# Optimization experiments

Measured on AMD Instinct MI355X. Metric: run time of the kernel, lower is better.

## Reference

```python
import jax, jax.numpy as jnp
import numpy as np
from jax import lax

B, C, H, W = 64, 512, 14, 14
HEAD_DIM = 32
NUM_HEADS = C // HEAD_DIM
HIDDEN = int(C * 4.0)
EPS = 1e-5
LS_INIT = 1e-5


def setup_inputs() -> dict:
    key = jax.random.key(0)
    ks = jax.random.split(key, 16)
    d = {}
    d['x'] = jax.random.normal(ks[0], (B, C, H, W), dtype=jnp.float32)
    # shared BatchNorm2d(dim) (inference-mode, running stats)
    d['bn_g'] = 1.0 + 0.1 * jax.random.normal(ks[1], (C,), dtype=jnp.float32)
    d['bn_b'] = 0.1 * jax.random.normal(ks[2], (C,), dtype=jnp.float32)
    d['bn_m'] = 0.1 * jax.random.normal(ks[3], (C,), dtype=jnp.float32)
    d['bn_v'] = jax.random.uniform(ks[4], (C,), minval=0.5, maxval=1.5, dtype=jnp.float32)
    # MHSA params (qkv_bias=False)
    d['qkv_w'] = 0.02 * jax.random.normal(ks[5], (3 * C, C), dtype=jnp.float32)
    d['proj_w'] = 0.02 * jax.random.normal(ks[6], (C, C), dtype=jnp.float32)
    d['proj_b'] = jnp.zeros((C,), dtype=jnp.float32)
    # ConvFFN: depthwise 7x7 (groups=C, no bias) -> BN -> 1x1 -> GELU -> 1x1
    d['dw_w'] = 0.02 * jax.random.normal(ks[7], (C, 1, 7, 7), dtype=jnp.float32)
    d['fbn_g'] = 1.0 + 0.1 * jax.random.normal(ks[8], (C,), dtype=jnp.float32)
    d['fbn_b'] = 0.1 * jax.random.normal(ks[9], (C,), dtype=jnp.float32)
    d['fbn_m'] = 0.1 * jax.random.normal(ks[10], (C,), dtype=jnp.float32)
    d['fbn_v'] = jax.random.uniform(ks[11], (C,), minval=0.5, maxval=1.5, dtype=jnp.float32)
    d['fc1_w'] = 0.02 * jax.random.normal(ks[12], (HIDDEN, C), dtype=jnp.float32)
    d['fc1_b'] = jnp.zeros((HIDDEN,), dtype=jnp.float32)
    d['fc2_w'] = 0.02 * jax.random.normal(ks[13], (C, HIDDEN), dtype=jnp.float32)
    d['fc2_b'] = jnp.zeros((C,), dtype=jnp.float32)
    # layer scale params, shape (C,1,1)
    d['ls1'] = LS_INIT * jnp.ones((C, 1, 1), dtype=jnp.float32)
    d['ls2'] = LS_INIT * jnp.ones((C, 1, 1), dtype=jnp.float32)
    return d


def _bn2d(x, g, b, m, v):
    # inference BatchNorm2d over channel dim of NCHW
    inv = g * lax.rsqrt(v + EPS)
    return x * inv[None, :, None, None] + (b - m * inv)[None, :, None, None]


def _mhsa(x, qkv_w, proj_w, proj_b):
    b, c, h, w = x.shape
    n = h * w
    xt = x.reshape(b, c, n).transpose(0, 2, 1)              # [B,N,C]
    qkv = xt @ qkv_w.T                                       # [B,N,3C]
    qkv = qkv.reshape(b, n, 3, NUM_HEADS, HEAD_DIM).transpose(2, 0, 3, 1, 4)
    q, k, v = qkv[0], qkv[1], qkv[2]                         # [B,h,N,d]
    scale = HEAD_DIM ** -0.5
    attn = jax.nn.softmax(jnp.einsum('bhnd,bhmd->bhnm', q * scale, k), axis=-1)
    o = jnp.einsum('bhnm,bhmd->bhnd', attn, v)               # [B,h,N,d]
    o = o.transpose(0, 2, 1, 3).reshape(b, n, c)             # [B,N,C]
    o = o @ proj_w.T + proj_b
    return o.transpose(0, 2, 1).reshape(b, c, h, w)


def _convffn(x, dw_w, fbn_g, fbn_b, fbn_m, fbn_v, fc1_w, fc1_b, fc2_w, fc2_b):
    y = lax.conv_general_dilated(x, dw_w, window_strides=(1, 1),
                                 padding=[(3, 3), (3, 3)],
                                 feature_group_count=C,
                                 dimension_numbers=('NCHW', 'OIHW', 'NCHW'))
    y = _bn2d(y, fbn_g, fbn_b, fbn_m, fbn_v)
    y = jnp.einsum('bchw,oc->bohw', y, fc1_w) + fc1_b[None, :, None, None]
    y = jax.nn.gelu(y, approximate=False)
    y = jnp.einsum('bchw,oc->bohw', y, fc2_w) + fc2_b[None, :, None, None]
    return y


def reference(x, bn_g, bn_b, bn_m, bn_v, qkv_w, proj_w, proj_b,
              dw_w, fbn_g, fbn_b, fbn_m, fbn_v, fc1_w, fc1_b, fc2_w, fc2_b,
              ls1, ls2):
    xn = _bn2d(x, bn_g, bn_b, bn_m, bn_v)
    x = x + ls1[None] * _mhsa(xn, qkv_w, proj_w, proj_b)
    xn = _bn2d(x, bn_g, bn_b, bn_m, bn_v)
    x = x + ls2[None] * _convffn(xn, dw_w, fbn_g, fbn_b, fbn_m, fbn_v,
                                 fc1_w, fc1_b, fc2_w, fc2_b)
    return x
```

## Files before the change

### kernel.cpp

```cpp
#include <hip/hip_runtime.h>
#include <hip/hip_bf16.h>
#include <hip/hip_fp8.h>
#include <stdint.h>

#define NTOK 196
#define NB   64
#define CCH  512
#define HID  2048
#define MTOT (NB * NTOK)

typedef __attribute__((ext_vector_type(8))) short  short8v;
typedef __attribute__((ext_vector_type(4))) float  float4v;
typedef __attribute__((ext_vector_type(2))) int    int2v;


__device__ __forceinline__ void mfma_fp8(float4v& d, int2v a, int2v b) {
  asm("v_mfma_f32_16x16x32_fp8_fp8 %0, %1, %2, %0" : "+v"(d) : "v"(a), "v"(b));
}

__device__ __forceinline__ void gload_lds16(const void* gsrc, void* ldst) {
  __builtin_amdgcn_global_load_lds(
      (const __attribute__((address_space(1))) unsigned int*)gsrc,
      (__attribute__((address_space(3))) unsigned int*)ldst, 16, 0, 0);
}

__device__ __forceinline__ int swz4(int r) { return (r ^ (r >> 2)) & 3; }

__device__ __forceinline__ uint32_t cvt2_fp8(float a, float b) {
  uint32_t d;
  asm("v_cvt_pk_fp8_f32 %0, %1, %2" : "=v"(d) : "v"(a), "v"(b));
  return d;
}


__global__ void prep_consts(const float* __restrict__ bn_g, const float* __restrict__ bn_b,
                            const float* __restrict__ bn_m, const float* __restrict__ bn_v,
                            const float* __restrict__ fbn_g, const float* __restrict__ fbn_b,
                            const float* __restrict__ fbn_m, const float* __restrict__ fbn_v,
                            float* __restrict__ cst) {
  int c = blockIdx.x * blockDim.x + threadIdx.x;
  if (c < CCH) {
    float i1 = bn_g[c] * rsqrtf(bn_v[c] + 1e-5f);
    cst[c] = i1;
    cst[512 + c] = bn_b[c] - bn_m[c] * i1;
    float i2 = fbn_g[c] * rsqrtf(fbn_v[c] + 1e-5f);
    cst[1024 + c] = i2;
    cst[1536 + c] = fbn_b[c] - fbn_m[c] * i2;
  }
}


__global__ void cvt_weights(const float* __restrict__ qkv_w, const float* __restrict__ proj_w,
                            const float* __restrict__ fc1_w, const float* __restrict__ fc2_w,
                            uint8_t* __restrict__ qkvb, uint8_t* __restrict__ projb,
                            uint8_t* __restrict__ fc1b, uint8_t* __restrict__ fc2b) {
  int i4 = blockIdx.x * blockDim.x + threadIdx.x;
  const int nq = 1536 * 512 / 4;
  const int np = 512 * 512 / 4;
  const int n1 = 2048 * 512 / 4;
  const float* src;
  uint8_t* dst;
  int k;
  if (i4 < nq)                { src = qkv_w;  dst = qkvb;  k = i4; }
  else if (i4 < nq + np)      { src = proj_w; dst = projb; k = i4 - nq; }
  else if (i4 < nq + np + n1) { src = fc1_w;  dst = fc1b;  k = i4 - nq - np; }
  else                        { src = fc2_w;  dst = fc2b;  k = i4 - nq - np - n1; }
  float4v v = *(const float4v*)(src + 4 * (size_t)k);
  uint32_t w0 = cvt2_fp8(v[0] * 16.0f, v[1] * 16.0f);
  uint32_t w1 = cvt2_fp8(v[2] * 16.0f, v[3] * 16.0f);
  *(uint16_t*)(dst + 4 * (size_t)k)     = (uint16_t)w0;
  *(uint16_t*)(dst + 4 * (size_t)k + 2) = (uint16_t)w1;
}


__global__ __launch_bounds__(256) void transpose_x(
    const float* __restrict__ x, uint8_t* __restrict__ xnt8,
    __hip_bfloat16* __restrict__ xt, const float* __restrict__ cst) {
  __shared__ float tile[32][33];
  const int n0 = blockIdx.x * 32;
  const int c0 = blockIdx.y * 32;
  const int b  = blockIdx.z;
  const int j = threadIdx.x & 31, i = threadIdx.x >> 5;
  #pragma unroll
  for (int p = 0; p < 4; ++p) {
    int cc = c0 + i + p * 8;
    int n = n0 + j;
    if (n < NTOK) tile[i + p * 8][j] = x[((size_t)b * CCH + cc) * NTOK + n];
  }
  __syncthreads();
  const float s = cst[c0 + j], t = cst[512 + c0 + j];
  float bn[4];
  size_t off[4];
  bool ok[4];
  #pragma unroll
  for (int p = 0; p < 4; ++p) {
    int n = n0 + i + p * 8;
    int cc = c0 + j;
    ok[p] = (n < NTOK);
    if (ok[p]) {
      float raw = tile[j][i + p * 8];
      size_t o = ((size_t)b * NTOK + n) * CCH + cc;
      xt[o] = __float2bfloat16(raw);
      bn[p] = raw * s + t;
      off[p] = o;
    }
  }
  uint32_t w0 = cvt2_fp8(bn[0], bn[1]);
  uint32_t w1 = cvt2_fp8(bn[2], bn[3]);
  if (ok[0]) xnt8[off[0]] = (uint8_t)w0;
  if (ok[1]) xnt8[off[1]] = (uint8_t)(w0 >> 8);
  if (ok[2]) xnt8[off[2]] = (uint8_t)w1;
  if (ok[3]) xnt8[off[3]] = (uint8_t)(w1 >> 8);
}


template<int EPI>
__global__ __launch_bounds__(256, 3) void gemm8f(
    const uint8_t* __restrict__ A, const uint8_t* __restrict__ Bw,
    int N, int K, int NY,
    __hip_bfloat16* __restrict__ outb, uint8_t* __restrict__ out8,
    const float* __restrict__ bias, const float* __restrict__ ls,
    const __hip_bfloat16* __restrict__ resid) {
  __shared__ char lds[49152];
  const int tid  = threadIdx.x;
  const int lane = tid & 63;
  const int wave = tid >> 6;

  const int q    = (int)gridDim.x >> 3;
  const int orig = blockIdx.x;
  const int wgid = (orig & 7) * q + (orig >> 3);
  const int bx = wgid / NY;
  const int by = wgid - bx * NY;

  const int m0 = bx * 128;
  const int n0 = by * 128;
  const int wm = (wave >> 1) * 64;
  const int wn = (wave & 1) * 64;
  const int KT = K >> 6;

  float4v acc[4][4] = {};

  auto stage = [&](int buf, int kt) {
    const int kb = kt * 64;
    char* base = lds + buf * 16384;
    #pragma unroll
    for (int i = 0; i < 2; ++i) {
      int L = i * 4096 + tid * 16;
      int row = L >> 6;
      int lc = ((L >> 4) & 3) ^ swz4(row);
      gload_lds16(A + (size_t)(m0 + row) * K + kb + lc * 16, base + L);
    }
    #pragma unroll
    for (int i = 0; i < 2; ++i) {
      int L = i * 4096 + tid * 16;
      int row = L >> 6;
      int lc = ((L >> 4) & 3) ^ swz4(row);
      gload_lds16(Bw + (size_t)(n0 + row) * K + kb + lc * 16, base + 8192 + L);
    }
  };

  auto compute = [&](int buf) {
    const char* bA = lds + buf * 16384;
    const char* bB = bA + 8192;
    const int g = lane >> 4;
    #pragma unroll
    for (int t = 0; t < 2; ++t) {
      int2v av[4], bv[4];
      #pragma unroll
      for (int f = 0; f < 4; ++f) {
        int row = wm + f * 16 + (lane & 15);
        int c16 = ((t << 1) | (g >> 1)) ^ swz4(row);
        av[f] = *(const int2v*)(bA + row * 64 + c16 * 16 + (g & 1) * 8);
      }
      #pragma unroll
      for (int j = 0; j < 4; ++j) {
        int row = wn + j * 16 + (lane & 15);
        int c16 = ((t << 1) | (g >> 1)) ^ swz4(row);
        bv[j] = *(const int2v*)(bB + row * 64 + c16 * 16 + (g & 1) * 8);
      }
      #pragma unroll
      for (int i = 0; i < 4; ++i)
        #pragma unroll
        for (int j = 0; j < 4; ++j)
          mfma_fp8(acc[i][j], av[i], bv[j]);
    }
  };

  stage(0, 0);
  stage(1, 1);
  int cur = 0;
  for (int kt = 0; kt < KT - 1; ++kt) {
    asm volatile("s_waitcnt vmcnt(4)" ::: "memory");
    __builtin_amdgcn_s_barrier();
    __builtin_amdgcn_sched_barrier(0);
    if (kt + 2 < KT) {
      int s = cur + 2; if (s >= 3) s -= 3;
      stage(s, kt + 2);
    }
    compute(cur);
    ++cur; if (cur == 3) cur = 0;
  }
  asm volatile("s_waitcnt vmcnt(0)" ::: "memory");
  __builtin_amdgcn_s_barrier();
  __builtin_amdgcn_sched_barrier(0);
  compute(cur);
  asm volatile("s_nop 7\n\ts_nop 7");

  const float RS = 0.0625f;

  if (EPI == 0) {
    #pragma unroll
    for (int i = 0; i < 4; ++i)
      #pragma unroll
      for (int j = 0; j < 4; ++j)
        #pragma unroll
        for (int r = 0; r < 4; r += 2) {
          int m = m0 + wm + i * 16 + ((lane >> 4) << 2) + r;
          int n = n0 + wn + j * 16 + (lane & 15);
          int bb = m / NTOK, tok = m - bb * NTOK;
          int bb2 = (m + 1) / NTOK, tok2 = (m + 1) - bb2 * NTOK;
          int sel = n >> 9, hh = (n >> 5) & 15, d = n & 31;
          uint32_t w = cvt2_fp8(acc[i][j][r] * RS, acc[i][j][r + 1] * RS);
          out8[(((size_t)(sel * 16 + hh) * NB + bb) * NTOK + tok) * 32 + d]  = (uint8_t)w;
          out8[(((size_t)(sel * 16 + hh) * NB + bb2) * NTOK + tok2) * 32 + d] = (uint8_t)(w >> 8);
        }
  } else {
    #pragma unroll
    for (int i = 0; i < 4; ++i)
      #pragma unroll
      for (int j = 0; j < 4; ++j)
        #pragma unroll
        for (int r = 0; r < 4; ++r) {
          int m = m0 + wm + i * 16 + ((lane >> 4) << 2) + r;
          int n = n0 + wn + j * 16 + (lane & 15);
          float v = acc[i][j][r] * RS + bias[n];
          v = __bfloat162float(resid[(size_t)m * CCH + n]) + ls[n] * v;
          outb[(size_t)m * CCH + n] = __float2bfloat16(v);
        }
  }
}


__global__ __launch_bounds__(512, 1) void ffn_fused(
    const uint8_t* __restrict__ yt8, const uint8_t* __restrict__ w1,
    const uint8_t* __restrict__ w2, const float* __restrict__ b1,
    const float* __restrict__ b2, const float* __restrict__ ls2,
    const __hip_bfloat16* __restrict__ resid, float* __restrict__ outf) {
  __shared__ char lds[131072];
  char* sA = lds;
  char* sH = lds + 32768;
  char* sB = lds + 65536;
  const int tid  = threadIdx.x;
  const int lane = tid & 63;
  const int wv   = tid >> 6;
  const int g    = lane >> 4;
  const int l15  = lane & 15;
  const int m0   = blockIdx.x * 64;
  const float RS = 0.0625f;

  #pragma unroll
  for (int u = 0; u < 4; ++u) {
    int L = u * 8192 + tid * 16;
    int r = L >> 9;
    int pc = (L >> 4) & 31;
    int lc = pc ^ (r & 31);
    gload_lds16(yt8 + (size_t)(m0 + r) * 512 + lc * 16, sA + L);
  }

  auto stageB = [&](const uint8_t* W, int rs, int kb, int buf) {
    char* base = sB + buf * 32768;
    #pragma unroll
    for (int u = 0; u < 4; ++u) {
      int L = u * 8192 + tid * 16;
      int r = L >> 6;
      int pc = (L >> 4) & 3;
      int lc = pc ^ swz4(r);
      gload_lds16(W + (size_t)r * rs + kb + lc * 16, base + L);
    }
  };

  auto step = [&](const char* Asrc, int ks, int buf, float4v (&acc)[4][4]) {
    const char* bB = sB + buf * 32768;
    #pragma unroll
    for (int t = 0; t < 2; ++t) {
      int2v av[4], bv[4];
      #pragma unroll
      for (int f = 0; f < 4; ++f) {
        int r = f * 16 + l15;
        int c = ks * 4 + t * 2 + (g >> 1);
        int pc = c ^ (r & 31);
        av[f] = *(const int2v*)(Asrc + r * 512 + pc * 16 + (g & 1) * 8);
      }
      #pragma unroll
      for (int j = 0; j < 4; ++j) {
        int r = wv * 64 + j * 16 + l15;
        int c16 = ((t << 1) | (g >> 1)) ^ swz4(r);
        bv[j] = *(const int2v*)(bB + r * 64 + c16 * 16 + (g & 1) * 8);
      }
      #pragma unroll
      for (int f = 0; f < 4; ++f)
        #pragma unroll
        for (int j = 0; j < 4; ++j)
          mfma_fp8(acc[f][j], av[f], bv[j]);
    }
  };

  float4v acc2[4][4] = {};

  stageB(w1, 512, 0, 0);
  __syncthreads();
  int par = 0;

  #pragma unroll 1
  for (int nh = 0; nh < 4; ++nh) {
    const uint8_t* W1c = w1 + (size_t)nh * 512 * 512;
    float4v acc1[4][4] = {};
    #pragma unroll 1
    for (int ks = 0; ks < 8; ++ks) {
      if (ks < 7) stageB(W1c, 512, (ks + 1) * 64, par ^ 1);
      else        stageB(w2, 2048, nh * 512, par ^ 1);
      step(sA, ks, par, acc1);
      __syncthreads();
      par ^= 1;
    }
    #pragma unroll
    for (int i = 0; i < 4; ++i)
      #pragma unroll
      for (int j = 0; j < 4; ++j) {
        int n = wv * 64 + j * 16 + l15;
        float bias1 = b1[nh * 512 + n];
        #pragma unroll
        for (int r = 0; r < 4; r += 2) {
          int m = i * 16 + (g << 2) + r;
          float z0 = acc1[i][j][r] * RS + bias1;
          float z1 = acc1[i][j][r + 1] * RS + bias1;
          float g0 = z0 / (1.0f + __expf(-1.702f * z0));
          float g1 = z1 / (1.0f + __expf(-1.702f * z1));
          uint32_t w = cvt2_fp8(g0, g1);
          int pc0 = ((n >> 4) ^ (m & 31)) * 16 + (n & 15);
          int pc1 = ((n >> 4) ^ ((m + 1) & 31)) * 16 + (n & 15);
          sH[m * 512 + pc0]       = (uint8_t)w;
          sH[(m + 1) * 512 + pc1] = (uint8_t)(w >> 8);
        }
      }
    __syncthreads();
    #pragma unroll 1
    for (int ks = 0; ks < 8; ++ks) {
      if (ks < 7)      stageB(w2, 2048, nh * 512 + (ks + 1) * 64, par ^ 1);
      else if (nh < 3) stageB(w1 + (size_t)(nh + 1) * 512 * 512, 512, 0, par ^ 1);
      step(sH, ks, par, acc2);
      __syncthreads();
      par ^= 1;
    }
  }
  asm volatile("s_nop 7\n\ts_nop 7");

  #pragma unroll 1
  for (int p = 0; p < 2; ++p) {
    __syncthreads();
    if ((wv >> 2) == p) {
      float* LT = (float*)(lds + (wv & 3) * 17408);
      #pragma unroll
      for (int i = 0; i < 4; ++i)
        #pragma unroll
        for (int j = 0; j < 4; ++j)
          #pragma unroll
          for (int r = 0; r < 4; ++r) {
            int ml = i * 16 + (g << 2) + r;
            int nl = j * 16 + l15;
            int n2 = wv * 64 + nl;
            float v = acc2[i][j][r] * RS + b2[n2];
            v = __bfloat162float(resid[(size_t)(m0 + ml) * CCH + n2]) + ls2[n2] * v;
            LT[nl * 68 + ml] = v;
          }
    }
    __syncthreads();
    #pragma unroll
    for (int u = 0; u < 8; ++u) {
      int idx = tid + 512 * u;
      int s = idx >> 10;
      int nl = (idx >> 4) & 63;
      int mq = idx & 15;
      const float* LT = (const float*)(lds + s * 17408);
      float4v v4 = *(const float4v*)(LT + nl * 68 + mq * 4);
      int n2 = (p * 4 + s) * 64 + nl;
      int m = m0 + mq * 4;
      int bb = m / NTOK, tok = m - bb * NTOK;
      *(float4v*)(outf + (size_t)bb * (CCH * NTOK) + (size_t)n2 * NTOK + tok) = v4;
    }
  }
}


__global__ __launch_bounds__(256, 3) void attn_kernel(
    const uint8_t* __restrict__ qkv8, uint8_t* __restrict__ o_t8) {
  __shared__ char sQ[208 * 48];
  __shared__ char sK[224 * 48];
  __shared__ char sV[32 * 240];
  __shared__ char sP[4][16 * 232];
  const int tid  = threadIdx.x;
  const int lane = tid & 63;
  const int wave = tid >> 6;
  const int b = blockIdx.x >> 4;
  const int h = blockIdx.x & 15;
  const size_t CHB = 6272;
  const uint8_t* Qg = qkv8 + ((size_t)(0 * 16 + h) * NB + b) * CHB;
  const uint8_t* Kg = qkv8 + ((size_t)(1 * 16 + h) * NB + b) * CHB;
  const uint8_t* Vg = qkv8 + ((size_t)(2 * 16 + h) * NB + b) * CHB;

  for (int i = tid; i < 144; i += 256) {
    int r = i / 12, w = i % 12;
    ((uint32_t*)(sQ + (196 + r) * 48))[w] = 0u;
  }
  for (int i = tid; i < 336; i += 256) {
    int r = i / 12, w = i % 12;
    ((uint32_t*)(sK + (196 + r) * 48))[w] = 0u;
  }
  for (int i = tid; i < 352; i += 256) {
    int d = i / 11, w = i % 11;
    ((uint32_t*)(sV + d * 240 + 196))[w] = 0u;
  }

  for (int c = tid; c < 392; c += 256) {
    int row = c >> 1, hf = c & 1;
    uint4 vq = *(const uint4*)(Qg + c * 16);
    *(uint4*)(sQ + row * 48 + hf * 16) = vq;
    uint4 vk = *(const uint4*)(Kg + c * 16);
    *(uint4*)(sK + row * 48 + hf * 16) = vk;
  }
  for (int u = tid; u < 784; u += 256) {
    int row = u >> 2, d0 = (u & 3) * 8;
    uint64_t w = *(const uint64_t*)(Vg + (size_t)u * 8);
    #pragma unroll
    for (int e = 0; e < 8; ++e)
      sV[(d0 + e) * 240 + row] = (char)(w >> (8 * e));
  }
  __syncthreads();

  const float scale = 0.17677669529663687f;
  char* Pw = sP[wave];
  const int g = lane >> 4;

  for (int mt = wave; mt < 13; mt += 4) {
    int qrow = mt * 16 + (lane & 15);
    int2v aq = *(const int2v*)(sQ + qrow * 48 + g * 8);

    float4v s[14];
    #pragma unroll
    for (int nt = 0; nt < 14; ++nt) {
      int krow = nt * 16 + (lane & 15);
      int2v bk = *(const int2v*)(sK + krow * 48 + g * 8);
      s[nt] = float4v{0.f, 0.f, 0.f, 0.f};
      mfma_fp8(s[nt], aq, bk);
    }
    asm volatile("s_nop 7\n\ts_nop 7");

    float mx[4] = {-INFINITY, -INFINITY, -INFINITY, -INFINITY};
    #pragma unroll
    for (int nt = 0; nt < 14; ++nt) {
      bool valid = (nt * 16 + (lane & 15)) < NTOK;
      #pragma unroll
      for (int r = 0; r < 4; ++r) {
        float v = valid ? s[nt][r] * scale : -INFINITY;
        s[nt][r] = v;
        mx[r] = fmaxf(mx[r], v);
      }
    }
    #pragma unroll
    for (int off = 1; off < 16; off <<= 1) {
      #pragma unroll
      for (int r = 0; r < 4; ++r) mx[r] = fmaxf(mx[r], __shfl_xor(mx[r], off));
    }
    float sum[4] = {0.f, 0.f, 0.f, 0.f};
    #pragma unroll
    for (int nt = 0; nt < 14; ++nt) {
      #pragma unroll
      for (int r = 0; r < 4; ++r) {
        float e = __expf(s[nt][r] - mx[r]);
        s[nt][r] = e;
        sum[r] += e;
      }
    }
    #pragma unroll
    for (int off = 1; off < 16; off <<= 1) {
      #pragma unroll
      for (int r = 0; r < 4; ++r) sum[r] += __shfl_xor(sum[r], off);
    }
    float rs[4];
    #pragma unroll
    for (int r = 0; r < 4; ++r) rs[r] = 1.0f / sum[r];

    #pragma unroll
    for (int nt = 0; nt < 14; ++nt) {
      int col = nt * 16 + (lane & 15);
      #pragma unroll
      for (int r = 0; r < 4; r += 2) {
        int prow = ((lane >> 4) << 2) + r;
        uint32_t w = cvt2_fp8(s[nt][r], s[nt][r + 1]);
        *(uint8_t*)(Pw + prow * 232 + col)       = (uint8_t)w;
        *(uint8_t*)(Pw + (prow + 1) * 232 + col) = (uint8_t)(w >> 8);
      }
    }

    float4v o0 = float4v{0.f, 0.f, 0.f, 0.f};
    float4v o1 = float4v{0.f, 0.f, 0.f, 0.f};
    #pragma unroll
    for (int ks = 0; ks < 7; ++ks) {
      int2v pa = *(const int2v*)(Pw + (lane & 15) * 232 + ks * 32 + g * 8);
      int2v v0 = *(const int2v*)(sV + (lane & 15) * 240 + ks * 32 + g * 8);
      int2v v1 = *(const int2v*)(sV + (16 + (lane & 15)) * 240 + ks * 32 + g * 8);
      mfma_fp8(o0, pa, v0);
      mfma_fp8(o1, pa, v1);
    }
    asm volatile("s_nop 7\n\ts_nop 7");

    #pragma unroll
    for (int r = 0; r < 4; ++r) {
      int trow = mt * 16 + ((lane >> 4) << 2) + r;
      if (trow < NTOK) {
        size_t ob = ((size_t)b * NTOK + trow) * CCH + h * 32 + (lane & 15);
        uint32_t w = cvt2_fp8(o0[r] * rs[r], o1[r] * rs[r]);
        o_t8[ob]      = (uint8_t)w;
        o_t8[ob + 16] = (uint8_t)(w >> 8);
      }
    }
  }
}


__global__ __launch_bounds__(448) void dwconv_tm(
    const __hip_bfloat16* __restrict__ x1t, const float* __restrict__ dw_w,
    const float* __restrict__ cst, uint8_t* __restrict__ yt8) {
  __shared__ float img[196][32];
  __shared__ float wgt[49][32];
  const int tid = threadIdx.x;
  const int b  = blockIdx.x >> 4;
  const int cb = (blockIdx.x & 15) * 32;
  const int c  = tid & 31;
  const int gc = cb + c;
  const float s = cst[gc], t0 = cst[512 + gc];
  #pragma unroll
  for (int k = 0; k < 14; ++k) {
    int p = (tid >> 5) + k * 14;
    img[p][c] = __bfloat162float(x1t[((size_t)b * NTOK + p) * CCH + gc]) * s + t0;
  }
  for (int i = tid; i < 49 * 32; i += 448) {
    int tap = i >> 5, cc = i & 31;
    wgt[tap][cc] = dw_w[(cb + cc) * 49 + tap];
  }
  __syncthreads();

  const int px = tid >> 5;
  float out[14];
  #pragma unroll
  for (int i = 0; i < 14; ++i) out[i] = 0.f;
  #pragma unroll 1
  for (int row = 0; row < 14; ++row) {
    float v[7];
    #pragma unroll
    for (int dx = 0; dx < 7; ++dx) {
      int ix = px + dx - 3;
      v[dx] = ((unsigned)ix < 14u) ? img[row * 14 + ix][c] : 0.f;
    }
    #pragma unroll
    for (int kk = 0; kk < 7; ++kk) {
      int py = row + 3 - kk;
      if (py >= 0 && py < 14) {
        float hsum = 0.f;
        #pragma unroll
        for (int dx = 0; dx < 7; ++dx) hsum = fmaf(v[dx], wgt[kk * 7 + dx][c], hsum);
        out[py] += hsum;
      }
    }
  }
  const float fs = cst[1024 + gc], ft = cst[1536 + gc];
  #pragma unroll
  for (int py = 0; py < 14; py += 2) {
    uint32_t w = cvt2_fp8(out[py] * fs + ft, out[py + 1] * fs + ft);
    yt8[((size_t)b * NTOK + py * 14 + px) * CCH + gc]       = (uint8_t)w;
    yt8[((size_t)b * NTOK + (py + 1) * 14 + px) * CCH + gc] = (uint8_t)(w >> 8);
  }
}


extern "C" void kernel_launch(void* const* d_in, const int* in_sizes, int n_in,
                              void* d_out, int out_size, void* d_ws, size_t ws_size,
                              hipStream_t stream) {
  const float* x      = (const float*)d_in[0];
  const float* bn_g   = (const float*)d_in[1];
  const float* bn_b   = (const float*)d_in[2];
  const float* bn_m   = (const float*)d_in[3];
  const float* bn_v   = (const float*)d_in[4];
  const float* qkv_w  = (const float*)d_in[5];
  const float* proj_w = (const float*)d_in[6];
  const float* proj_b = (const float*)d_in[7];
  const float* dw_w   = (const float*)d_in[8];
  const float* fbn_g  = (const float*)d_in[9];
  const float* fbn_b  = (const float*)d_in[10];
  const float* fbn_m  = (const float*)d_in[11];
  const float* fbn_v  = (const float*)d_in[12];
  const float* fc1_w  = (const float*)d_in[13];
  const float* fc1_b  = (const float*)d_in[14];
  const float* fc2_w  = (const float*)d_in[15];
  const float* fc2_b  = (const float*)d_in[16];
  const float* ls1    = (const float*)d_in[17];
  const float* ls2    = (const float*)d_in[18];

  char* ws = (char*)d_ws;
  float* cst             = (float*)ws;
  uint8_t* qkvb8         = (uint8_t*)(ws + 32768);
  uint8_t* projb8        = (uint8_t*)(ws + 819200);
  uint8_t* fc1b8         = (uint8_t*)(ws + 1081344);
  uint8_t* fc2b8         = (uint8_t*)(ws + 2129920);
  uint8_t* xnt8          = (uint8_t*)(ws + 3178496);
  __hip_bfloat16* xt     = (__hip_bfloat16*)(ws + 9601024);
  uint8_t* qkv8          = (uint8_t*)(ws + 22446080);
  uint8_t* ot8           = (uint8_t*)(ws + 60981248);
  __hip_bfloat16* x1t    = (__hip_bfloat16*)(ws + 67403776);
  uint8_t* yt8           = (uint8_t*)(ws + 80248832);

  prep_consts<<<dim3(2), dim3(256), 0, stream>>>(bn_g, bn_b, bn_m, bn_v,
                                                 fbn_g, fbn_b, fbn_m, fbn_v, cst);
  cvt_weights<<<dim3(3072), dim3(256), 0, stream>>>(qkv_w, proj_w, fc1_w, fc2_w,
                                                    qkvb8, projb8, fc1b8, fc2b8);
  transpose_x<<<dim3(7, 16, 64), dim3(256), 0, stream>>>(x, xnt8, xt, cst);
  gemm8f<0><<<dim3(1176), dim3(256), 0, stream>>>(xnt8, qkvb8, 1536, 512, 12,
                                                  nullptr, qkv8, nullptr, nullptr, nullptr);
  attn_kernel<<<dim3(1024), dim3(256), 0, stream>>>(qkv8, ot8);
  gemm8f<1><<<dim3(392), dim3(256), 0, stream>>>(ot8, projb8, 512, 512, 4,
                                                 x1t, nullptr, proj_b, ls1, xt);
  dwconv_tm<<<dim3(1024), dim3(448), 0, stream>>>(x1t, dw_w, cst, yt8);
  ffn_fused<<<dim3(196), dim3(512), 0, stream>>>(yt8, fc1b8, fc2b8, fc1_b, fc2_b,
                                                 ls2, x1t, (float*)d_out);
}
```

Measured before the change: 209.9 us.

## Triple-buffer weight staging in fused FFN with flattened 64-step pipeline

Replaces the double-buffered weight staging in the fused FFN kernel with a three-slot ring buffer. The nested fc1/fc2 loops become one 64-iteration loop that prefetches two steps ahead and uses vmcnt waits with a raw barrier instead of a full __syncthreads after every step. This aims to hide global-to-LDS load latency behind MFMA work. In exchange it grows LDS use to 160KB and depends on the hand-written vmcnt counts and barrier placement being correct, including ordering around the sH writes after the GELU.

After: 229.5 us. 1.09x slower.

```diff
diff --git a/kernel.cpp b/kernel.cpp
--- a/kernel.cpp
+++ b/kernel.cpp
@@ -246,7 +246,7 @@
     const uint8_t* __restrict__ w2, const float* __restrict__ b1,
     const float* __restrict__ b2, const float* __restrict__ ls2,
     const __hip_bfloat16* __restrict__ resid, float* __restrict__ outf) {
-  __shared__ char lds[131072];
+  __shared__ char lds[163840];
   char* sA = lds;
   char* sH = lds + 32768;
   char* sB = lds + 65536;
@@ -267,8 +267,8 @@
     gload_lds16(yt8 + (size_t)(m0 + r) * 512 + lc * 16, sA + L);
   }
 
-  auto stageB = [&](const uint8_t* W, int rs, int kb, int buf) {
-    char* base = sB + buf * 32768;
+  auto stageB = [&](const uint8_t* W, int rs, int kb, int slot) {
+    char* base = sB + slot * 32768;
     #pragma unroll
     for (int u = 0; u < 4; ++u) {
       int L = u * 8192 + tid * 16;
@@ -279,8 +279,14 @@
     }
   };
 
-  auto step = [&](const char* Asrc, int ks, int buf, float4v (&acc)[4][4]) {
-    const char* bB = sB + buf * 32768;
+  auto stage_for = [&](int k) {
+    int nh = k >> 4, s = k & 15;
+    if (s < 8) stageB(w1 + (size_t)nh * 262144, 512, s * 64, k % 3);
+    else       stageB(w2, 2048, nh * 512 + (s - 8) * 64, k % 3);
+  };
+
+  auto step = [&](const char* Asrc, int ks, int slot, float4v (&acc)[4][4]) {
+    const char* bB = sB + slot * 32768;
     #pragma unroll
     for (int t = 0; t < 2; ++t) {
       int2v av[4], bv[4];
@@ -305,52 +311,46 @@
     }
   };
 
+  float4v acc1[4][4] = {};
   float4v acc2[4][4] = {};
 
-  stageB(w1, 512, 0, 0);
-  __syncthreads();
-  int par = 0;
+  stage_for(0);
+  stage_for(1);
 
   #pragma unroll 1
-  for (int nh = 0; nh < 4; ++nh) {
-    const uint8_t* W1c = w1 + (size_t)nh * 512 * 512;
-    float4v acc1[4][4] = {};
-    #pragma unroll 1
-    for (int ks = 0; ks < 8; ++ks) {
-      if (ks < 7) stageB(W1c, 512, (ks + 1) * 64, par ^ 1);
-      else        stageB(w2, 2048, nh * 512, par ^ 1);
-      step(sA, ks, par, acc1);
-      __syncthreads();
-      par ^= 1;
-    }
-    #pragma unroll
-    for (int i = 0; i < 4; ++i)
-      #pragma unroll
-      for (int j = 0; j < 4; ++j) {
-        int n = wv * 64 + j * 16 + l15;
-        float bias1 = b1[nh * 512 + n];
+  for (int k = 0; k < 64; ++k) {
+    const int s = k & 15;
+    if (k + 1 < 64) asm volatile("s_waitcnt vmcnt(4)" ::: "memory");
+    else            asm volatile("s_waitcnt vmcnt(0)" ::: "memory");
+    __builtin_amdgcn_s_barrier();
+    __builtin_amdgcn_sched_barrier(0);
+    if (k + 2 < 64) stage_for(k + 2);
+    if (s < 8) step(sA, s, k % 3, acc1);
+    else       step(sH, s - 8, k % 3, acc2);
+    if (s == 7) {
+      const int nh = k >> 4;
+      #pragma unroll
+      for (int i = 0; i < 4; ++i)
         #pragma unroll
-        for (int r = 0; r < 4; r += 2) {
-          int m = i * 16 + (g << 2) + r;
-          float z0 = acc1[i][j][r] * RS + bias1;
-          float z1 = acc1[i][j][r + 1] * RS + bias1;
-          float g0 = z0 / (1.0f + __expf(-1.702f * z0));
-          float g1 = z1 / (1.0f + __expf(-1.702f * z1));
-          uint32_t w = cvt2_fp8(g0, g1);
-          int pc0 = ((n >> 4) ^ (m & 31)) * 16 + (n & 15);
-          int pc1 = ((n >> 4) ^ ((m + 1) & 31)) * 16 + (n & 15);
-          sH[m * 512 + pc0]       = (uint8_t)w;
-          sH[(m + 1) * 512 + pc1] = (uint8_t)(w >> 8);
+        for (int j = 0; j < 4; ++j) {
+          int n = wv * 64 + j * 16 + l15;
+          float bias1 = b1[nh * 512 + n];
+          #pragma unroll
+          for (int r = 0; r < 4; r += 2) {
+            int m = i * 16 + (g << 2) + r;
+            float z0 = acc1[i][j][r] * RS + bias1;
+            float z1 = acc1[i][j][r + 1] * RS + bias1;
+            float g0 = z0 / (1.0f + __expf(-1.702f * z0));
+            float g1 = z1 / (1.0f + __expf(-1.702f * z1));
+            uint32_t w = cvt2_fp8(g0, g1);
+            int pc0 = ((n >> 4) ^ (m & 31)) * 16 + (n & 15);
+            int pc1 = ((n >> 4) ^ ((m + 1) & 31)) * 16 + (n & 15);
+            sH[m * 512 + pc0]       = (uint8_t)w;
+            sH[(m + 1) * 512 + pc1] = (uint8_t)(w >> 8);
+            acc1[i][j][r] = 0.f;
+            acc1[i][j][r + 1] = 0.f;
+          }
         }
-      }
-    __syncthreads();
-    #pragma unroll 1
-    for (int ks = 0; ks < 8; ++ks) {
-      if (ks < 7)      stageB(w2, 2048, nh * 512 + (ks + 1) * 64, par ^ 1);
-      else if (nh < 3) stageB(w1 + (size_t)(nh + 1) * 512 * 512, 512, 0, par ^ 1);
-      step(sH, ks, par, acc2);
-      __syncthreads();
-      par ^= 1;
     }
   }
   asm volatile("s_nop 7\n\ts_nop 7");
```
